# Performance work log

Hardware: AMD Instinct MI355X
Metric: run time of the kernel (lower is better)

The kernel has to match this reference:

```python
import jax, jax.numpy as jnp
import numpy as np

GROUPSIZE = 4      # g: multivariate group size (d = groupsize - 2)
NB_GROUPS = 48     # f: number of expert groups / filters
CHANNELS = 128     # c: signal channels fed to the L operator
SCALE = 0.999
SLOPE = 1.0        # model_params['scaling']
LAMB_INIT = 0.1
EPS_OMEGA_INIT = -2.0


def proj_l1(x):
    """Euclidean projection onto the unit l1 ball along axis 1. x: [B,G,F,H,W]."""
    ax = jnp.abs(x)
    s = -jnp.sort(-ax, axis=1)                      # descending |x|
    cssv = jnp.cumsum(s, axis=1) - 1.0
    G = x.shape[1]
    k = jnp.arange(1, G + 1, dtype=x.dtype).reshape(1, G, 1, 1, 1)
    cond = s * k > cssv
    rho = jnp.sum(cond, axis=1, keepdims=True)       # number of active coords
    theta = jnp.take_along_axis(cssv, rho - 1, axis=1) / rho.astype(x.dtype)
    theta = jnp.maximum(theta, 0.0)
    proj = jnp.sign(x) * jnp.maximum(ax - theta, 0.0)
    inside = jnp.sum(ax, axis=1, keepdims=True) <= 1.0
    return jnp.where(inside, x, proj)


def _forward(x_noisy, sigma, Q_param, taus_param, lamb, eps_omega,
             mu_w1, mu_b1, mu_w2, mu_b2, mu_w3, mu_b3, Wf, n_iter):
    lamb_e = jnp.exp(lamb)
    eps_e = jnp.exp(eps_omega)

    # --- Q normalization + spectral norms (cached once per forward) ---
    Q = Q_param / jnp.maximum(jnp.sum(jnp.abs(Q_param), axis=2, keepdims=True), 1.0)
    Q_norms = jnp.linalg.svd(Q, compute_uv=False)[:, 0].reshape(-1, 1, 1)  # [F,1,1]
    Q_eff = Q / Q_norms ** 2
    taus = jnp.exp(jax.nn.relu(taus_param))          # [1,1,F,1,1]

    # --- per-batch noise-adaptive scaling via small MLP ---
    h = jax.nn.relu((sigma * 20.0 - 2.0) @ mu_w1 + mu_b1)
    h = jax.nn.relu(h @ mu_w2 + mu_b2)
    h = h @ mu_w3 + mu_b3                            # [B,F]
    scaling = jax.nn.relu(h * 0.05 + sigma) * SLOPE + 1e-9
    scaling = scaling.reshape(-1, 1, scaling.shape[-1], 1, 1)  # [B,1,F,1,1]

    def moreau(x):
        g = proj_l1(x)
        cost = jnp.max(jnp.abs(x - g), axis=1) + 0.5 * jnp.sum(g * g, axis=1)
        cost = cost[:, None]                         # [B,1,F,H,W]
        g = g + eps_e * x
        cost = cost + eps_e * 0.5 * jnp.sqrt(jnp.sum(x * x, axis=1, keepdims=True))
        return g, cost

    def activation(x):
        gc, cc = moreau(x)
        # orient: scale * einsum('flg,bgfhw->blfhw', Q/Q_norms^2, x), then /taus
        y = SCALE * jnp.einsum('flg,bgfhw->blfhw', Q_eff, x) / taus
        gcc, ccc = moreau(y)
        # unorient: scale * einsum with Q^T  (Q^T[f,l,g] = Q[f,g,l])
        gcc = SCALE * jnp.einsum('fgl,bgfhw->blfhw', Q, gcc)
        ccc = Q_norms ** 2 * (taus * ccc)
        return lamb_e * (gc - gcc), lamb_e * (cc - ccc)

    def reconstruct(x):
        Lx = jnp.einsum('gfc,bchw->bgfhw', Wf, x) / scaling
        g, cost = activation(Lx)
        g = jnp.einsum('gfc,bgfhw->bchw', Wf, g * scaling)   # adjoint L^T
        cost = jnp.sum(cost * scaling ** 2, axis=(1, 2, 3, 4))
        g = (x - x_noisy + g) / (1.0 + lamb_e * (1.0 + eps_e))
        cost = cost + 0.5 * jnp.sum((x - x_noisy) ** 2, axis=(1, 2, 3))
        return g, cost

    def step(x, _):
        g, _c = reconstruct(x)
        return x - g, None

    x_final, _ = jax.lax.scan(jax.checkpoint(step), x_noisy, jnp.arange(n_iter))
    return x_final


def setup_inputs() -> dict:
    key = jax.random.key(0)
    ks = jax.random.split(key, 8)
    B, C, H, W = 2, CHANNELS, 128, 128
    F_, G = NB_GROUPS, GROUPSIZE
    x_noisy = jax.random.normal(ks[0], (B, C, H, W), jnp.float32)
    sigma = jax.random.uniform(ks[1], (B, 1), jnp.float32)
    Q_param = jax.random.uniform(ks[2], (F_, G, G), jnp.float32) - 0.5
    taus_param = (LAMB_INIT / 2.0) * jnp.ones((1, 1, F_, 1, 1), jnp.float32)
    lamb = jnp.float32(LAMB_INIT)
    eps_omega = jnp.float32(EPS_OMEGA_INIT)
    mu_w1 = jax.random.normal(ks[3], (1, F_), jnp.float32)
    mu_b1 = jnp.zeros((F_,), jnp.float32)
    mu_w2 = jax.random.normal(ks[4], (F_, F_), jnp.float32) / np.float32(np.sqrt(F_))
    mu_b2 = jnp.zeros((F_,), jnp.float32)
    mu_w3 = jax.random.normal(ks[5], (F_, F_), jnp.float32) / np.float32(np.sqrt(F_))
    mu_b3 = jnp.zeros((F_,), jnp.float32)
    Wf = jax.random.normal(ks[6], (G, F_, C), jnp.float32) / np.float32(np.sqrt(C))
    return dict(x_noisy=x_noisy, sigma=sigma, Q_param=Q_param, taus_param=taus_param,
                lamb=lamb, eps_omega=eps_omega, mu_w1=mu_w1, mu_b1=mu_b1,
                mu_w2=mu_w2, mu_b2=mu_b2, mu_w3=mu_w3, mu_b3=mu_b3, Wf=Wf, n_iter=10)


def reference(x_noisy, sigma, Q_param, taus_param, lamb, eps_omega,
              mu_w1, mu_b1, mu_w2, mu_b2, mu_w3, mu_b3, Wf, n_iter):
    return _forward(x_noisy, sigma, Q_param, taus_param, lamb, eps_omega,
                    mu_w1, mu_b1, mu_w2, mu_b2, mu_w3, mu_b3, Wf, n_iter)
```

## Files before the change

### kernel.cpp

```cpp
#include <hip/hip_runtime.h>
#include <math.h>

#define F_ 48
#define C_ 128
#define HW 16384
#define SCALE_C 0.999f
#define TPB 256
#define MTPB 512

typedef __attribute__((ext_vector_type(4))) float floatx4;
typedef __attribute__((ext_vector_type(8))) _Float16 half8;
typedef __attribute__((ext_vector_type(4))) _Float16 half4;

#define P1_U 0
#define P2_U 49152
#define QEQN_F 49152
#define MISC_F (QEQN_F + 1536)
#define SINV_F (MISC_F + 2)
#define SLAM_F (SINV_F + 96)

__global__ void setup_math(const float* __restrict__ sigma,
                           const float* __restrict__ Qp,
                           const float* __restrict__ taus_p,
                           const float* __restrict__ lamb,
                           const float* __restrict__ eps_om,
                           const float* __restrict__ mw1, const float* __restrict__ mb1,
                           const float* __restrict__ mw2, const float* __restrict__ mb2,
                           const float* __restrict__ mw3, const float* __restrict__ mb3,
                           float* __restrict__ wsf)
{
    const int tid = threadIdx.x;
    if (tid < F_) {
        const int f = tid;
        float Qm[4][4];
        for (int g = 0; g < 4; ++g) {
            float s = 0.f;
            for (int l = 0; l < 4; ++l) s += fabsf(Qp[f * 16 + g * 4 + l]);
            float d = fmaxf(s, 1.0f);
            for (int l = 0; l < 4; ++l) Qm[g][l] = Qp[f * 16 + g * 4 + l] / d;
        }
        double A[4][4];
        for (int i = 0; i < 4; ++i)
            for (int j = 0; j < 4; ++j) {
                double s = 0.0;
                for (int g = 0; g < 4; ++g) s += (double)Qm[g][i] * (double)Qm[g][j];
                A[i][j] = s;
            }
        double M[4][4];
        for (int i = 0; i < 4; ++i) for (int j = 0; j < 4; ++j) M[i][j] = A[i][j];
        for (int it = 0; it < 30; ++it) {
            double T[4][4]; double mx = 0.0;
            for (int i = 0; i < 4; ++i)
                for (int j = 0; j < 4; ++j) {
                    double s = 0.0;
                    for (int k = 0; k < 4; ++k) s += M[i][k] * M[k][j];
                    T[i][j] = s;
                    double a = fabs(s); if (a > mx) mx = a;
                }
            if (mx < 1e-300) break;
            double inv = 1.0 / mx;
            for (int i = 0; i < 4; ++i) for (int j = 0; j < 4; ++j) M[i][j] = T[i][j] * inv;
        }
        int jb = 0; double bn = -1.0;
        for (int j = 0; j < 4; ++j) {
            double nn = 0.0;
            for (int i = 0; i < 4; ++i) nn += M[i][j] * M[i][j];
            if (nn > bn) { bn = nn; jb = j; }
        }
        double v[4]; for (int i = 0; i < 4; ++i) v[i] = M[i][jb];
        double Av[4];
        for (int i = 0; i < 4; ++i) {
            double s = 0.0;
            for (int j = 0; j < 4; ++j) s += A[i][j] * v[j];
            Av[i] = s;
        }
        double vv = 0.0, vav = 0.0;
        for (int i = 0; i < 4; ++i) { vv += v[i] * v[i]; vav += v[i] * Av[i]; }
        float lamf = (float)((vv > 0.0) ? (vav / vv) : 0.0);
        float tau = expf(fmaxf(taus_p[f], 0.0f));
        float qsv = SCALE_C / tau;
        for (int l = 0; l < 4; ++l)
            for (int g = 0; g < 4; ++g)
                wsf[QEQN_F + f * 32 + l * 4 + g] = qsv * Qm[l][g] / lamf;
        for (int g = 0; g < 4; ++g)
            for (int l = 0; l < 4; ++l)
                wsf[QEQN_F + f * 32 + 16 + g * 4 + l] = SCALE_C * Qm[g][l];
    }
    if (tid >= 48 && tid < 50) {
        const int b = tid - 48;
        float lamb_e = expf(lamb[0]);
        float sg = sigma[b];
        float t = sg * 20.0f - 2.0f;
        float h1[F_], h2[F_];
        for (int j = 0; j < F_; ++j) h1[j] = fmaxf(t * mw1[j] + mb1[j], 0.0f);
        for (int j = 0; j < F_; ++j) {
            float s = mb2[j];
            for (int k = 0; k < F_; ++k) s += h1[k] * mw2[k * F_ + j];
            h2[j] = fmaxf(s, 0.0f);
        }
        for (int j = 0; j < F_; ++j) {
            float s = mb3[j];
            for (int k = 0; k < F_; ++k) s += h2[k] * mw3[k * F_ + j];
            float sc = fmaxf(s * 0.05f + sg, 0.0f) + 1e-9f;
            wsf[SINV_F + b * F_ + j] = 1.0f / sc;
            wsf[SLAM_F + b * F_ + j] = lamb_e * sc;
        }
    }
    if (tid == 50) {
        float lamb_e = expf(lamb[0]);
        float eps_e = expf(eps_om[0]);
        wsf[MISC_F + 0] = eps_e;
        wsf[MISC_F + 1] = 1.0f / (1.0f + lamb_e * (1.0f + eps_e));
    }
}

__global__ void setup_pack(const float* __restrict__ Wf, float* __restrict__ wsf)
{
    unsigned short* wsu = (unsigned short*)wsf;
    const int gtid = blockIdx.x * TPB + threadIdx.x;
    for (int i = gtid; i < 98304; i += gridDim.x * TPB) {
        if (i < 49152) {
            int j = i & 7, lane = (i >> 3) & 63;
            int t = i >> 9;
            int ks = t & 3, mtile = t >> 2;
            int rt = lane & 15, qq = lane >> 4;
            int c = ks * 32 + qq * 8 + j;
            int ft = mtile >> 1;
            int f = ft * 4 + (rt >> 2);
            int gl = rt & 3;
            float w;
            if ((mtile & 1) == 0) {
                w = Wf[(gl * F_ + f) * C_ + c];
            } else {
                w = 0.f;
                for (int g = 0; g < 4; ++g)
                    w += wsf[QEQN_F + f * 32 + gl * 4 + g] * Wf[(g * F_ + f) * C_ + c];
            }
            _Float16 hv = (_Float16)w;
            wsu[P1_U + ((mtile * 4 + ks) * 64 + lane) * 8 + j] = *(unsigned short*)&hv;
        } else {
            int ii = i - 49152;
            int j = ii & 7, lane = (ii >> 3) & 63;
            int t = ii >> 9;
            int ks = t % 12, cmt = t / 12;
            int m = lane & 15, qq = lane >> 4;
            int cch = cmt * 16 + m;
            int r = ks * 32 + qq * 8 + j;
            float w;
            if (ks < 6) {
                int f = r >> 2, g = r & 3;
                w = Wf[(g * F_ + f) * C_ + cch];
            } else {
                int rp = r - 192;
                int f = rp >> 2, l = rp & 3;
                w = 0.f;
                for (int g = 0; g < 4; ++g)
                    w += wsf[QEQN_F + f * 32 + 16 + l * 4 + g] * Wf[(g * F_ + f) * C_ + cch];
                w = -w;
            }
            _Float16 hv = (_Float16)w;
            wsu[P2_U + ((cmt * 12 + ks) * 64 + lane) * 8 + j] = *(unsigned short*)&hv;
        }
    }
}

__device__ __forceinline__ void proj4(const float v[4], float o[4]) {
    float a0 = fabsf(v[0]), a1 = fabsf(v[1]), a2 = fabsf(v[2]), a3 = fabsf(v[3]);
    float sum = a0 + a1 + a2 + a3;
    float t0 = fmaxf(a0, a1), u0 = fminf(a0, a1);
    float t1 = fmaxf(a2, a3), u1 = fminf(a2, a3);
    float s0 = fmaxf(t0, t1), m0 = fminf(t0, t1);
    float m1 = fmaxf(u0, u1), s3 = fminf(u0, u1);
    float s1 = fmaxf(m1, m0), s2 = fminf(m1, m0);
    float c2 = s0 + s1, c3 = c2 + s2, c4 = c3 + s3;
    float th = s0 - 1.0f, rs = 1.0f;
    if (s1 * 2.0f > c2 - 1.0f) { th = c2 - 1.0f; rs = 0.5f; }
    if (s2 * 3.0f > c3 - 1.0f) { th = c3 - 1.0f; rs = (1.0f / 3.0f); }
    if (s3 * 4.0f > c4 - 1.0f) { th = c4 - 1.0f; rs = 0.25f; }
    float theta = fmaxf(th * rs, 0.0f);
    bool inside = (sum <= 1.0f);
#pragma unroll
    for (int g = 0; g < 4; ++g) {
        float ag = fabsf(v[g]);
        float pg = copysignf(fmaxf(ag - theta, 0.0f), v[g]);
        o[g] = inside ? v[g] : pg;
    }
}

__global__ __launch_bounds__(MTPB, 4) void mfoe_main(
    const float* __restrict__ xnoisy,
    const float* __restrict__ wsf,
    float* __restrict__ out,
    const int* __restrict__ n_iter_p)
{
    __shared__ __align__(16) _Float16 sXF[8192];
    __shared__ __align__(16) _Float16 sACT[24576];
    __shared__ __align__(16) float sISL[96];

    const int tid = threadIdx.x;
    const int lane = tid & 63;
    const int wv = __builtin_amdgcn_readfirstlane(tid >> 6);
    const int n = lane & 15;
    const int q = lane >> 4;
    const int blk = blockIdx.x;
    const int b = blk >> 8;
    const int pix0 = (blk & 255) << 6;

    const float* __restrict__ xin = xnoisy + b * (C_ * HW) + pix0;
    float* __restrict__ oimg = out + b * (C_ * HW) + pix0;
    const unsigned short* __restrict__ wsu = (const unsigned short*)wsf;
    const int niter = *n_iter_p;

    if (niter == 0) {
        for (int i = tid; i < C_ * 64; i += MTPB) {
            int p = i & 63, c = i >> 6;
            oimg[c * HW + p] = xin[c * HW + p];
        }
        return;
    }

    for (int i = tid; i < C_ * 64; i += MTPB) {
        int p = i & 63, c = i >> 6;
        int idx = (((p >> 4) * 4 + (c >> 5)) * 64 + ((c >> 3) & 3) * 16 + (p & 15)) * 8 + (c & 7);
        sXF[idx] = (_Float16)xin[c * HW + p];
    }
    for (int i = tid; i < 96; i += MTPB) {
        if (i < 48) sISL[i] = wsf[SINV_F + b * F_ + i];
        else        sISL[i] = wsf[SLAM_F + b * F_ + (i - 48)];
    }

    float xnr[16], xr[16];
#pragma unroll
    for (int np = 0; np < 4; ++np)
#pragma unroll
        for (int l = 0; l < 4; ++l) {
            float v = xin[(wv * 16 + q * 4 + l) * HW + np * 16 + n];
            xnr[np * 4 + l] = v;
            xr[np * 4 + l] = v;
        }
    const float eps_e = wsf[MISC_F + 0];
    const float invden = wsf[MISC_F + 1];

    for (int it = 0; it < niter; ++it) {
        __syncthreads();
#pragma unroll 1
        for (int jj = 0; jj < 3; ++jj) {
            int grp = wv * 3 + jj, ft = grp >> 1, nph = grp & 1;
            int np0 = nph * 2;
            floatx4 accv0 = (floatx4){0.f, 0.f, 0.f, 0.f};
            floatx4 accv1 = (floatx4){0.f, 0.f, 0.f, 0.f};
            floatx4 accy0 = (floatx4){0.f, 0.f, 0.f, 0.f};
            floatx4 accy1 = (floatx4){0.f, 0.f, 0.f, 0.f};
            const half8* aE = (const half8*)(wsu + P1_U + (ft * 8) * 512 + lane * 8);
            const half8* b0 = (const half8*)&sXF[(np0 * 4) * 512 + lane * 8];
            const half8* b1 = (const half8*)&sXF[((np0 + 1) * 4) * 512 + lane * 8];
#pragma unroll
            for (int ks = 0; ks < 4; ++ks) {
                half8 aV = aE[ks * 64];
                half8 aY = aE[ks * 64 + 256];
                half8 bF0 = b0[ks * 64];
                half8 bF1 = b1[ks * 64];
                accv0 = __builtin_amdgcn_mfma_f32_16x16x32_f16(aV, bF0, accv0, 0, 0, 0);
                accy0 = __builtin_amdgcn_mfma_f32_16x16x32_f16(aY, bF0, accy0, 0, 0, 0);
                accv1 = __builtin_amdgcn_mfma_f32_16x16x32_f16(aV, bF1, accv1, 0, 0, 0);
                accy1 = __builtin_amdgcn_mfma_f32_16x16x32_f16(aY, bF1, accy1, 0, 0, 0);
            }
            int f = ft * 4 + q;
            float invs = sISL[f];
            float slam = sISL[48 + f];
#pragma unroll
            for (int h = 0; h < 2; ++h) {
                int np = np0 + h;
                floatx4 accv = h ? accv1 : accv0;
                floatx4 accy = h ? accy1 : accy0;
                float v[4] = {accv[0] * invs, accv[1] * invs, accv[2] * invs, accv[3] * invs};
                float y[4] = {accy[0] * invs, accy[1] * invs, accy[2] * invs, accy[3] * invs};
                float pv[4]; proj4(v, pv);
                float py[4]; proj4(y, py);
                half4 au, am;
#pragma unroll
                for (int g = 0; g < 4; ++g) {
                    au[g] = (_Float16)(fmaf(eps_e, v[g], pv[g]) * slam);
                    am[g] = (_Float16)(fmaf(eps_e, y[g], py[g]) * slam);
                }
                int aw = ((np * 12 + (ft >> 1)) * 64 + ((ft & 1) * 2 + (q >> 1)) * 16 + n) * 8 + (q & 1) * 4;
                *(half4*)&sACT[aw] = au;
                *(half4*)&sACT[aw + 3072] = am;
            }
        }
        __syncthreads();
        floatx4 acc2[4];
#pragma unroll
        for (int np = 0; np < 4; ++np) acc2[np] = (floatx4){0.f, 0.f, 0.f, 0.f};
        {
            const half8* a2F = (const half8*)(wsu + P2_U + (wv * 12) * 512 + lane * 8);
            const half8* bAp = (const half8*)&sACT[lane * 8];
#pragma unroll
            for (int ks = 0; ks < 12; ++ks) {
                half8 aF = a2F[ks * 64];
#pragma unroll
                for (int np = 0; np < 4; ++np) {
                    half8 bA = bAp[(np * 12 + ks) * 64];
                    acc2[np] = __builtin_amdgcn_mfma_f32_16x16x32_f16(aF, bA, acc2[np], 0, 0, 0);
                }
            }
        }
        const bool last = (it == niter - 1);
#pragma unroll
        for (int np = 0; np < 4; ++np) {
            int p = np * 16 + n;
            half4 nx4;
#pragma unroll
            for (int l = 0; l < 4; ++l) {
                float xo = xr[np * 4 + l];
                float nx = xo - ((xo - xnr[np * 4 + l]) + acc2[np][l]) * invden;
                xr[np * 4 + l] = nx;
                nx4[l] = (_Float16)nx;
                if (last) oimg[(wv * 16 + q * 4 + l) * HW + p] = nx;
            }
            int xu = ((np * 4 + (wv >> 1)) * 64 + ((wv & 1) * 2 + (q >> 1)) * 16 + n) * 8 + (q & 1) * 4;
            *(half4*)&sXF[xu] = nx4;
        }
    }
}

extern "C" void kernel_launch(void* const* d_in, const int* in_sizes, int n_in,
                              void* d_out, int out_size, void* d_ws, size_t ws_size,
                              hipStream_t stream) {
    const float* x_noisy = (const float*)d_in[0];
    const float* sigma   = (const float*)d_in[1];
    const float* Qp      = (const float*)d_in[2];
    const float* taus_p  = (const float*)d_in[3];
    const float* lamb    = (const float*)d_in[4];
    const float* eps_om  = (const float*)d_in[5];
    const float* mw1     = (const float*)d_in[6];
    const float* mb1     = (const float*)d_in[7];
    const float* mw2     = (const float*)d_in[8];
    const float* mb2     = (const float*)d_in[9];
    const float* mw3     = (const float*)d_in[10];
    const float* mb3     = (const float*)d_in[11];
    const float* Wf      = (const float*)d_in[12];
    const int*   n_iter  = (const int*)d_in[13];
    float* out = (float*)d_out;
    float* ws  = (float*)d_ws;

    hipLaunchKernelGGL(setup_math, dim3(1), dim3(64), 0, stream,
                       sigma, Qp, taus_p, lamb, eps_om,
                       mw1, mb1, mw2, mb2, mw3, mb3, ws);
    hipLaunchKernelGGL(setup_pack, dim3(192), dim3(TPB), 0, stream, Wf, ws);
    hipLaunchKernelGGL(mfoe_main, dim3(512), dim3(MTPB), 0, stream,
                       x_noisy, ws, out, n_iter);
}
```

Measured before the change: 283.7 us.

## Restructure stage-one MFMA loop to reuse X fragments across three filter tiles

Measured after the change: 470.3 us. 1.66x slower.

```diff
diff --git a/kernel.cpp b/kernel.cpp
--- a/kernel.cpp
+++ b/kernel.cpp
@@ -195,7 +195,6 @@
 {
     __shared__ __align__(16) _Float16 sXF[8192];
     __shared__ __align__(16) _Float16 sACT[24576];
-    __shared__ __align__(16) float sISL[96];
 
     const int tid = threadIdx.x;
     const int lane = tid & 63;
@@ -224,57 +223,80 @@
         int idx = (((p >> 4) * 4 + (c >> 5)) * 64 + ((c >> 3) & 3) * 16 + (p & 15)) * 8 + (c & 7);
         sXF[idx] = (_Float16)xin[c * HW + p];
     }
-    for (int i = tid; i < 96; i += MTPB) {
-        if (i < 48) sISL[i] = wsf[SINV_F + b * F_ + i];
-        else        sISL[i] = wsf[SLAM_F + b * F_ + (i - 48)];
-    }
-
-    float xnr[16], xr[16];
+
+    const int ftg = wv >> 1;
+    const int nph = wv & 1;
+
+    float invsr[3], slamr[3];
+#pragma unroll
+    for (int t = 0; t < 3; ++t) {
+        int f = (ftg * 3 + t) * 4 + q;
+        invsr[t] = wsf[SINV_F + b * F_ + f];
+        slamr[t] = wsf[SLAM_F + b * F_ + f];
+    }
+    float xnr[16];
 #pragma unroll
     for (int np = 0; np < 4; ++np)
 #pragma unroll
-        for (int l = 0; l < 4; ++l) {
-            float v = xin[(wv * 16 + q * 4 + l) * HW + np * 16 + n];
-            xnr[np * 4 + l] = v;
-            xr[np * 4 + l] = v;
-        }
+        for (int l = 0; l < 4; ++l)
+            xnr[np * 4 + l] = xin[(wv * 16 + q * 4 + l) * HW + np * 16 + n];
+
     const float eps_e = wsf[MISC_F + 0];
     const float invden = wsf[MISC_F + 1];
 
+    const half8* __restrict__ A1 = (const half8*)wsu;
+    const half8* __restrict__ A2 = (const half8*)(wsu + P2_U);
+    const half8* __restrict__ sXF8 = (const half8*)sXF;
+    const half8* __restrict__ sACT8 = (const half8*)sACT;
+
     for (int it = 0; it < niter; ++it) {
         __syncthreads();
-#pragma unroll 1
-        for (int jj = 0; jj < 3; ++jj) {
-            int grp = wv * 3 + jj, ft = grp >> 1, nph = grp & 1;
-            int np0 = nph * 2;
-            floatx4 accv0 = (floatx4){0.f, 0.f, 0.f, 0.f};
-            floatx4 accv1 = (floatx4){0.f, 0.f, 0.f, 0.f};
-            floatx4 accy0 = (floatx4){0.f, 0.f, 0.f, 0.f};
-            floatx4 accy1 = (floatx4){0.f, 0.f, 0.f, 0.f};
-            const half8* aE = (const half8*)(wsu + P1_U + (ft * 8) * 512 + lane * 8);
-            const half8* b0 = (const half8*)&sXF[(np0 * 4) * 512 + lane * 8];
-            const half8* b1 = (const half8*)&sXF[((np0 + 1) * 4) * 512 + lane * 8];
-#pragma unroll
-            for (int ks = 0; ks < 4; ++ks) {
-                half8 aV = aE[ks * 64];
-                half8 aY = aE[ks * 64 + 256];
-                half8 bF0 = b0[ks * 64];
-                half8 bF1 = b1[ks * 64];
-                accv0 = __builtin_amdgcn_mfma_f32_16x16x32_f16(aV, bF0, accv0, 0, 0, 0);
-                accy0 = __builtin_amdgcn_mfma_f32_16x16x32_f16(aY, bF0, accy0, 0, 0, 0);
-                accv1 = __builtin_amdgcn_mfma_f32_16x16x32_f16(aV, bF1, accv1, 0, 0, 0);
-                accy1 = __builtin_amdgcn_mfma_f32_16x16x32_f16(aY, bF1, accy1, 0, 0, 0);
-            }
-            int f = ft * 4 + q;
-            float invs = sISL[f];
-            float slam = sISL[48 + f];
+        floatx4 av[3][2], ay[3][2];
+#pragma unroll
+        for (int t = 0; t < 3; ++t)
 #pragma unroll
             for (int h = 0; h < 2; ++h) {
-                int np = np0 + h;
-                floatx4 accv = h ? accv1 : accv0;
-                floatx4 accy = h ? accy1 : accy0;
-                float v[4] = {accv[0] * invs, accv[1] * invs, accv[2] * invs, accv[3] * invs};
-                float y[4] = {accy[0] * invs, accy[1] * invs, accy[2] * invs, accy[3] * invs};
+                av[t][h] = (floatx4){0.f, 0.f, 0.f, 0.f};
+                ay[t][h] = (floatx4){0.f, 0.f, 0.f, 0.f};
+            }
+#pragma unroll
+        for (int ks = 0; ks < 4; ++ks) {
+            half8 aV0 = A1[(((ftg * 3 + 0) * 2 + 0) * 4 + ks) * 64 + lane];
+            half8 aY0 = A1[(((ftg * 3 + 0) * 2 + 1) * 4 + ks) * 64 + lane];
+            half8 aV1 = A1[(((ftg * 3 + 1) * 2 + 0) * 4 + ks) * 64 + lane];
+            half8 aY1 = A1[(((ftg * 3 + 1) * 2 + 1) * 4 + ks) * 64 + lane];
+            half8 aV2 = A1[(((ftg * 3 + 2) * 2 + 0) * 4 + ks) * 64 + lane];
+            half8 aY2 = A1[(((ftg * 3 + 2) * 2 + 1) * 4 + ks) * 64 + lane];
+            half8 b0 = sXF8[((nph * 2 + 0) * 4 + ks) * 64 + lane];
+            half8 b1 = sXF8[((nph * 2 + 1) * 4 + ks) * 64 + lane];
+            av[0][0] = __builtin_amdgcn_mfma_f32_16x16x32_f16(aV0, b0, av[0][0], 0, 0, 0);
+            ay[0][0] = __builtin_amdgcn_mfma_f32_16x16x32_f16(aY0, b0, ay[0][0], 0, 0, 0);
+            av[0][1] = __builtin_amdgcn_mfma_f32_16x16x32_f16(aV0, b1, av[0][1], 0, 0, 0);
+            ay[0][1] = __builtin_amdgcn_mfma_f32_16x16x32_f16(aY0, b1, ay[0][1], 0, 0, 0);
+            av[1][0] = __builtin_amdgcn_mfma_f32_16x16x32_f16(aV1, b0, av[1][0], 0, 0, 0);
+            ay[1][0] = __builtin_amdgcn_mfma_f32_16x16x32_f16(aY1, b0, ay[1][0], 0, 0, 0);
+            av[1][1] = __builtin_amdgcn_mfma_f32_16x16x32_f16(aV1, b1, av[1][1], 0, 0, 0);
+            ay[1][1] = __builtin_amdgcn_mfma_f32_16x16x32_f16(aY1, b1, ay[1][1], 0, 0, 0);
+            av[2][0] = __builtin_amdgcn_mfma_f32_16x16x32_f16(aV2, b0, av[2][0], 0, 0, 0);
+            ay[2][0] = __builtin_amdgcn_mfma_f32_16x16x32_f16(aY2, b0, ay[2][0], 0, 0, 0);
+            av[2][1] = __builtin_amdgcn_mfma_f32_16x16x32_f16(aV2, b1, av[2][1], 0, 0, 0);
+            ay[2][1] = __builtin_amdgcn_mfma_f32_16x16x32_f16(aY2, b1, ay[2][1], 0, 0, 0);
+        }
+        half8 a2[4];
+#pragma unroll
+        for (int k = 0; k < 4; ++k) a2[k] = A2[(wv * 12 + k) * 64 + lane];
+#pragma unroll
+        for (int t = 0; t < 3; ++t) {
+            const float invs = invsr[t];
+            const float slam = slamr[t];
+            const int ft = ftg * 3 + t;
+#pragma unroll
+            for (int h = 0; h < 2; ++h) {
+                const int np = nph * 2 + h;
+                float v[4] = {av[t][h][0] * invs, av[t][h][1] * invs,
+                              av[t][h][2] * invs, av[t][h][3] * invs};
+                float y[4] = {ay[t][h][0] * invs, ay[t][h][1] * invs,
+                              ay[t][h][2] * invs, ay[t][h][3] * invs};
                 float pv[4]; proj4(v, pv);
                 float py[4]; proj4(y, py);
                 half4 au, am;
@@ -292,33 +314,32 @@
         floatx4 acc2[4];
 #pragma unroll
         for (int np = 0; np < 4; ++np) acc2[np] = (floatx4){0.f, 0.f, 0.f, 0.f};
-        {
-            const half8* a2F = (const half8*)(wsu + P2_U + (wv * 12) * 512 + lane * 8);
-            const half8* bAp = (const half8*)&sACT[lane * 8];
-#pragma unroll
-            for (int ks = 0; ks < 12; ++ks) {
-                half8 aF = a2F[ks * 64];
-#pragma unroll
-                for (int np = 0; np < 4; ++np) {
-                    half8 bA = bAp[(np * 12 + ks) * 64];
-                    acc2[np] = __builtin_amdgcn_mfma_f32_16x16x32_f16(aF, bA, acc2[np], 0, 0, 0);
-                }
-            }
+#pragma unroll
+        for (int ks = 0; ks < 12; ++ks) {
+            half8 aF = (ks < 4) ? a2[ks] : A2[(wv * 12 + ks) * 64 + lane];
+            half8 bA0 = sACT8[(0 * 12 + ks) * 64 + lane];
+            half8 bA1 = sACT8[(1 * 12 + ks) * 64 + lane];
+            half8 bA2 = sACT8[(2 * 12 + ks) * 64 + lane];
+            half8 bA3 = sACT8[(3 * 12 + ks) * 64 + lane];
+            acc2[0] = __builtin_amdgcn_mfma_f32_16x16x32_f16(aF, bA0, acc2[0], 0, 0, 0);
+            acc2[1] = __builtin_amdgcn_mfma_f32_16x16x32_f16(aF, bA1, acc2[1], 0, 0, 0);
+            acc2[2] = __builtin_amdgcn_mfma_f32_16x16x32_f16(aF, bA2, acc2[2], 0, 0, 0);
+            acc2[3] = __builtin_amdgcn_mfma_f32_16x16x32_f16(aF, bA3, acc2[3], 0, 0, 0);
         }
         const bool last = (it == niter - 1);
 #pragma unroll
         for (int np = 0; np < 4; ++np) {
             int p = np * 16 + n;
+            int xu = ((np * 4 + (wv >> 1)) * 64 + ((wv & 1) * 2 + (q >> 1)) * 16 + n) * 8 + (q & 1) * 4;
+            half4 xo4 = *(const half4*)&sXF[xu];
             half4 nx4;
 #pragma unroll
             for (int l = 0; l < 4; ++l) {
-                float xo = xr[np * 4 + l];
+                float xo = (float)xo4[l];
                 float nx = xo - ((xo - xnr[np * 4 + l]) + acc2[np][l]) * invden;
-                xr[np * 4 + l] = nx;
                 nx4[l] = (_Float16)nx;
                 if (last) oimg[(wv * 16 + q * 4 + l) * HW + p] = nx;
             }
-            int xu = ((np * 4 + (wv >> 1)) * 64 + ((wv & 1) * 2 + (q >> 1)) * 16 + n) * 8 + (q & 1) * 4;
             *(half4*)&sXF[xu] = nx4;
         }
     }
```
